# Performance work log

Measured on AMD Instinct MI355X. Metric: run time of the kernel, lower is better.

The kernel has to match this reference:

```python
import jax, jax.numpy as jnp
import numpy as np

N_NODES = 100000
N_EDGES = 1600000
F_IN, HID, N_CLS = 128, 64, 40


def gcn_conv(x, src, dst, W, b, n_nodes):
    # x: [N, Fin] -> [N, Fout]; edges already include self-loops.
    h = x @ W  # [N, Fout]
    ones = jnp.ones_like(src, dtype=h.dtype)
    deg = jax.ops.segment_sum(ones, dst, num_segments=n_nodes)  # [N]
    dinv = jnp.where(deg > 0, jax.lax.rsqrt(deg), 0.0)
    norm = dinv[src] * dinv[dst]  # [E]
    msg = h[src] * norm[:, None]  # gather + scale
    out = jax.ops.segment_sum(msg, dst, num_segments=n_nodes)  # scatter-sum
    return out + b


def setup_inputs() -> dict:
    key = jax.random.key(0)
    ks = jax.random.split(key, 8)
    x = jax.random.normal(ks[0], (N_NODES, F_IN), dtype=jnp.float32)
    edge_index = jax.random.randint(ks[1], (2, N_EDGES), 0, N_NODES, dtype=jnp.int64)

    def glorot(k, fi, fo):
        s = float(np.sqrt(6.0 / (fi + fo)))
        return jax.random.uniform(k, (fi, fo), jnp.float32, -s, s)

    return {
        "x": x,
        "edge_index": edge_index,
        "W1": glorot(ks[2], F_IN, HID), "b1": jnp.zeros((HID,), jnp.float32),
        "W2": glorot(ks[3], HID, HID), "b2": jnp.zeros((HID,), jnp.float32),
        "W3": glorot(ks[4], HID, N_CLS), "b3": jnp.zeros((N_CLS,), jnp.float32),
    }


def reference(x, edge_index, W1, b1, W2, b2, W3, b3):
    n = x.shape[0]
    loop = jnp.arange(n, dtype=edge_index.dtype)
    src = jnp.concatenate([edge_index[0], loop])  # add self-loops
    dst = jnp.concatenate([edge_index[1], loop])
    # layer 1..3: GCNConv -> relu -> dropout(eval: identity)
    h = jax.nn.relu(gcn_conv(x, src, dst, W1, b1, n))
    h = jax.nn.relu(gcn_conv(h, src, dst, W2, b2, n))
    h = jax.nn.relu(gcn_conv(h, src, dst, W3, b3, n))
    return jax.nn.log_softmax(h, axis=1)
```

## Files before the change

### kernel.cpp

```cpp
#include <hip/hip_runtime.h>
#include <math.h>

typedef _Float16 half8   __attribute__((ext_vector_type(8)));
typedef float    float4v __attribute__((ext_vector_type(4)));

#define CAP   6144
#define EPB   8192

static __device__ __forceinline__ unsigned short f32_to_f16u(float f) {
    _Float16 h = (_Float16)f;
    return __builtin_bit_cast(unsigned short, h);
}


__global__ __launch_bounds__(256) void prep_init(
    const float* __restrict__ W1, const float* __restrict__ W2, const float* __restrict__ W3,
    unsigned short* __restrict__ Wf1, unsigned short* __restrict__ Wf2,
    unsigned short* __restrict__ Wf3, int* __restrict__ bcur, int NB)
{
    if (blockIdx.x == 3) {
        for (int i = threadIdx.x; i < NB; i += 256) bcur[i] = 0;
        return;
    }
    const float* W; unsigned short* Wf; int K, M;
    if (blockIdx.x == 0)      { W = W1; Wf = Wf1; K = 128; M = 64; }
    else if (blockIdx.x == 1) { W = W2; Wf = Wf2; K = 64;  M = 64; }
    else                      { W = W3; Wf = Wf3; K = 64;  M = 40; }
    const int NT = (M + 15) >> 4, NTC = NT << 4, KS = K >> 5;
    for (int i = threadIdx.x; i < K * NTC; i += 256) {
        int k = i / NTC, nn = i - k * NTC;
        unsigned short hv = 0;
        if (nn < M) hv = f32_to_f16u(W[(size_t)k * M + nn]);
        int s = k >> 5, q = (k >> 3) & 3, j = k & 7;
        int u = nn >> 4, lane = (q << 4) | (nn & 15);
        Wf[((u * KS + s) << 9) + (lane << 3) + j] = hv;
    }
}


__global__ __launch_bounds__(256) void bin_edges(
    const int* __restrict__ src, const int* __restrict__ dst,
    int* __restrict__ bcur, unsigned int* __restrict__ bint, int E, int NB)
{
    __shared__ unsigned int pay[EPB];
    __shared__ unsigned int targ[EPB];
    __shared__ int h[512];
    __shared__ int h2[512];
    __shared__ int sc[512];
    __shared__ int rbase[512];

    const int tid  = threadIdx.x;
    const int base = (int)blockIdx.x * EPB;
    int end = base + EPB; if (end > E) end = E;
    const int total = end - base;
    const int L4 = total & ~3;

    h[tid] = 0; h[tid + 256] = 0;
    h2[tid] = 0; h2[tid + 256] = 0;
    __syncthreads();

    for (int i = tid << 2; i < L4; i += 1024) {
        int4 d4 = *(const int4*)(dst + base + i);
        atomicAdd(&h[d4.x >> 8], 1);
        atomicAdd(&h[d4.y >> 8], 1);
        atomicAdd(&h[d4.z >> 8], 1);
        atomicAdd(&h[d4.w >> 8], 1);
    }
    for (int i = L4 + tid; i < total; i += 256)
        atomicAdd(&h[dst[base + i] >> 8], 1);
    __syncthreads();

    int v0 = h[tid], v1 = h[tid + 256];
    sc[tid] = v0; sc[tid + 256] = v1;
    __syncthreads();
    for (int off = 1; off < 512; off <<= 1) {
        int x0 = (tid >= off) ? sc[tid - off] : 0;
        int x1 = (tid + 256 >= off) ? sc[tid + 256 - off] : 0;
        __syncthreads();
        sc[tid] += x0; sc[tid + 256] += x1;
        __syncthreads();
    }

    for (int j = tid; j < NB; j += 256) {
        int c = h[j];
        rbase[j] = c ? atomicAdd(&bcur[j], c) : 0;
    }
    __syncthreads();

    {
        auto place = [&](int d, int s) {
            int bkt  = d >> 8;
            int rank = atomicAdd(&h2[bkt], 1);
            int loc  = sc[bkt] - h[bkt] + rank;
            pay[loc] = ((unsigned int)s << 8) | (unsigned int)(d & 255);
            unsigned int t = (unsigned int)(rbase[bkt] + rank);
            targ[loc] = (t < (unsigned int)CAP)
                      ? (unsigned int)bkt * CAP + t : 0xFFFFFFFFu;
        };
        for (int i = tid << 2; i < L4; i += 1024) {
            int4 d4 = *(const int4*)(dst + base + i);
            int4 s4 = *(const int4*)(src + base + i);
            place(d4.x, s4.x); place(d4.y, s4.y);
            place(d4.z, s4.z); place(d4.w, s4.w);
        }
        for (int i = L4 + tid; i < total; i += 256)
            place(dst[base + i], src[base + i]);
    }
    __syncthreads();

    for (int i = tid; i < total; i += 256) {
        unsigned int t = targ[i];
        if (t != 0xFFFFFFFFu) bint[t] = pay[i];
    }
}


__global__ __launch_bounds__(256) void build_csr(
    const unsigned int* __restrict__ bint, const int* __restrict__ bcur,
    int2* __restrict__ rp2, float* __restrict__ dinv, int* __restrict__ es, int n)
{
    __shared__ int cnt[256];
    __shared__ int sc[256];
    __shared__ int cur[256];
    __shared__ unsigned int pin[CAP];
    __shared__ int pout[CAP];
    const int b = blockIdx.x, tid = threadIdx.x;
    int total = bcur[b]; if (total > CAP) total = CAP;
    const unsigned int* bp = bint + (size_t)b * CAP;
    int* ep = es + (size_t)b * CAP;
    const int base = b * CAP;

    cnt[tid] = 0;
    __syncthreads();
    for (int i = tid; i < total; i += 256) {
        unsigned int v = bp[i];
        pin[i] = v;
        atomicAdd(&cnt[v & 255], 1);
    }
    __syncthreads();

    int v = cnt[tid];
    sc[tid] = v;
    __syncthreads();
    for (int off = 1; off < 256; off <<= 1) {
        int x = (tid >= off) ? sc[tid - off] : 0;
        __syncthreads();
        sc[tid] += x;
        __syncthreads();
    }
    int excl = sc[tid] - v;
    int node = (b << 8) + tid;
    if (node < n) {
        rp2[node]  = make_int2(base + excl, base + excl + v);
        dinv[node] = rsqrtf((float)(v + 1));
    }
    cur[tid] = excl;
    __syncthreads();

    for (int i = tid; i < total; i += 256) {
        unsigned int p = pin[i];
        int r = atomicAdd(&cur[p & 255], 1);
        pout[r] = (int)(p >> 8);
    }
    __syncthreads();

    for (int i = tid; i < total; i += 256)
        ep[i] = pout[i];
}


template<int KK, int NT, int STRIDE, int MOUT, bool INF32>
__global__ __launch_bounds__(256) void gemm_t(
    const void* __restrict__ Xin, const unsigned short* __restrict__ Wf,
    const float* __restrict__ dinv, unsigned short* __restrict__ H, int n)
{
    constexpr int KS = KK >> 5;
    __shared__ __align__(16) unsigned short ldsA[4 * KS * 512];
    const int tid = threadIdx.x;
    const int n0  = blockIdx.x * 64;
    const int wv   = tid >> 6;
    const int lane = tid & 63;

    half8 bf[NT * KS];
    #pragma unroll
    for (int u = 0; u < NT; ++u)
        #pragma unroll
        for (int s = 0; s < KS; ++s)
            bf[u * KS + s] = *(const half8*)&Wf[((u * KS + s) << 9) + (lane << 3)];

    {
        const int rl = tid >> 3;
        const int kl = tid & 7;
        #pragma unroll
        for (int rb = 0; rb < 64; rb += 32) {
            int r = rl + rb;
            int node = n0 + r;
            int t = r >> 4, m = r & 15;
            if (INF32) {
                #pragma unroll
                for (int kq8 = 0; kq8 < (KK >> 2); kq8 += 8) {
                    int k0 = (kl + kq8) << 2;
                    unsigned short h[4] = {0, 0, 0, 0};
                    if (node < n) {
                        const float* xp = (const float*)Xin + (size_t)node * KK + k0;
                        float4v v = *(const float4v*)xp;
                        #pragma unroll
                        for (int i = 0; i < 4; ++i) h[i] = f32_to_f16u(v[i]);
                    }
                    int s = k0 >> 5, q = (k0 >> 3) & 3, j0 = k0 & 7;
                    int lds_lane = (q << 4) | m;
                    unsigned short* p = &ldsA[((t * KS + s) << 9) + (lds_lane << 3) + j0];
                    *(uint2*)p = make_uint2((unsigned)h[0] | ((unsigned)h[1] << 16),
                                            (unsigned)h[2] | ((unsigned)h[3] << 16));
                }
            } else {
                uint4 v = make_uint4(0, 0, 0, 0);
                if (node < n)
                    v = *(const uint4*)((const unsigned short*)Xin + (size_t)node * KK + (kl << 3));
                int k0 = kl << 3;
                int s = k0 >> 5, q = (k0 >> 3) & 3;
                unsigned short* p = &ldsA[((t * KS + s) << 9) + ((((q << 4) | m)) << 3)];
                *(uint4*)p = v;
            }
        }
    }

    __syncthreads();

    float4v acc[NT];
    #pragma unroll
    for (int u = 0; u < NT; ++u) acc[u] = (float4v){0.f, 0.f, 0.f, 0.f};

    #pragma unroll
    for (int s = 0; s < KS; ++s) {
        half8 a = *(const half8*)&ldsA[((wv * KS + s) << 9) + (lane << 3)];
        #pragma unroll
        for (int u = 0; u < NT; ++u)
            acc[u] = __builtin_amdgcn_mfma_f32_16x16x32_f16(a, bf[u * KS + s], acc[u], 0, 0, 0);
    }

    const int mc = lane & 15;
    const int quad = lane >> 4;
    #pragma unroll
    for (int reg = 0; reg < 4; ++reg) {
        int node = n0 + (wv << 4) + (quad << 2) + reg;
        if (node >= n) continue;
        float dv = dinv[node];
        #pragma unroll
        for (int u = 0; u < NT; ++u) {
            int col = (u << 4) + mc;
            if (col < MOUT)
                H[(size_t)node * STRIDE + col] = f32_to_f16u(acc[u][reg] * dv);
        }
    }
}


template<int MOUT, int ROWU4>
__global__ __launch_bounds__(256) void gather_t(
    const int2* __restrict__ rp2, const int* __restrict__ es,
    const unsigned short* __restrict__ H, const float* __restrict__ dinv,
    const float* __restrict__ bias, unsigned short* __restrict__ Aout, int n)
{
    const int lane   = threadIdx.x & 63;
    const int half   = lane >> 5;
    const int lane32 = lane & 31;
    const int slot   = (lane >> 3) & 3;
    const int c8     = lane & 7;
    const bool act   = c8 < ROWU4;
    const uint4* H4  = (const uint4*)H;

    float bi[8];
    #pragma unroll
    for (int i = 0; i < 8; ++i) bi[i] = bias[(c8 << 3) + i];

    const half8 hz = {(_Float16)0, (_Float16)0, (_Float16)0, (_Float16)0,
                      (_Float16)0, (_Float16)0, (_Float16)0, (_Float16)0};

    const int TW2 = (int)(gridDim.x << 3);
    for (int nb = (((int)blockIdx.x << 2) + ((int)threadIdx.x >> 6)) << 1; nb < n; nb += TW2) {
        const int node = nb + half;
        const int2 e = rp2[node];
        const float dv = dinv[node];

        half8 hacc = hz;
        if (slot == 0 && act)
            hacc = __builtin_bit_cast(half8, H4[(size_t)node * ROWU4 + c8]);

        for (int cb = e.x; cb < e.y; cb += 32) {
            const int rem = e.y - cb;
            int eidx = cb + lane32; if (eidx > e.y - 1) eidx = e.y - 1;
            const int ei = es[eidx];
            #pragma unroll
            for (int j = 0; j < 8; ++j) {
                const int idx = (j << 2) + slot;
                const int s = __shfl(ei, (half << 5) + idx, 64);
                if (idx < rem && act)
                    hacc = hacc + __builtin_bit_cast(half8, H4[(size_t)s * ROWU4 + c8]);
            }
        }

        #pragma unroll
        for (int step = 8; step <= 16; step <<= 1) {
            uint4 u = __builtin_bit_cast(uint4, hacc);
            uint4 o;
            o.x = __shfl_xor(u.x, step, 64);
            o.y = __shfl_xor(u.y, step, 64);
            o.z = __shfl_xor(u.z, step, 64);
            o.w = __shfl_xor(u.w, step, 64);
            hacc = hacc + __builtin_bit_cast(half8, o);
        }

        if (slot == 0) {
            unsigned short o[8];
            #pragma unroll
            for (int i = 0; i < 8; ++i)
                o[i] = f32_to_f16u(fmaxf((float)hacc[i] * dv + bi[i], 0.0f));
            uint4 w;
            w.x = (unsigned int)o[0] | ((unsigned int)o[1] << 16);
            w.y = (unsigned int)o[2] | ((unsigned int)o[3] << 16);
            w.z = (unsigned int)o[4] | ((unsigned int)o[5] << 16);
            w.w = (unsigned int)o[6] | ((unsigned int)o[7] << 16);
            ((uint4*)Aout)[(size_t)node * 8 + c8] = w;
        }
    }
}


template<int MOUT, int ROWU4>
__global__ __launch_bounds__(256) void gather_softmax(
    const int2* __restrict__ rp2, const int* __restrict__ es,
    const unsigned short* __restrict__ H, const float* __restrict__ dinv,
    const float* __restrict__ bias, float* __restrict__ out, int n)
{
    const int lane   = threadIdx.x & 63;
    const int half   = lane >> 5;
    const int lane32 = lane & 31;
    const int slot   = (lane >> 3) & 3;
    const int c8     = lane & 7;
    const bool act   = c8 < ROWU4;
    const uint4* H4  = (const uint4*)H;

    float bi[8];
    #pragma unroll
    for (int i = 0; i < 8; ++i) {
        int col = (c8 << 3) + i;
        bi[i] = (col < MOUT) ? bias[col] : 0.0f;
    }

    const half8 hz = {(_Float16)0, (_Float16)0, (_Float16)0, (_Float16)0,
                      (_Float16)0, (_Float16)0, (_Float16)0, (_Float16)0};

    const int TW2 = (int)(gridDim.x << 3);
    for (int nb = (((int)blockIdx.x << 2) + ((int)threadIdx.x >> 6)) << 1; nb < n; nb += TW2) {
        const int node = nb + half;
        const int2 e = rp2[node];
        const float dv = dinv[node];

        half8 hacc = hz;
        if (slot == 0 && act)
            hacc = __builtin_bit_cast(half8, H4[(size_t)node * ROWU4 + c8]);

        for (int cb = e.x; cb < e.y; cb += 32) {
            const int rem = e.y - cb;
            int eidx = cb + lane32; if (eidx > e.y - 1) eidx = e.y - 1;
            const int ei = es[eidx];
            #pragma unroll
            for (int j = 0; j < 8; ++j) {
                const int idx = (j << 2) + slot;
                const int s = __shfl(ei, (half << 5) + idx, 64);
                if (idx < rem && act)
                    hacc = hacc + __builtin_bit_cast(half8, H4[(size_t)s * ROWU4 + c8]);
            }
        }

        #pragma unroll
        for (int step = 8; step <= 16; step <<= 1) {
            uint4 u = __builtin_bit_cast(uint4, hacc);
            uint4 o;
            o.x = __shfl_xor(u.x, step, 64);
            o.y = __shfl_xor(u.y, step, 64);
            o.z = __shfl_xor(u.z, step, 64);
            o.w = __shfl_xor(u.w, step, 64);
            hacc = hacc + __builtin_bit_cast(half8, o);
        }

        float z[8]; float m = -INFINITY;
        #pragma unroll
        for (int i = 0; i < 8; ++i) {
            int col = (c8 << 3) + i;
            z[i] = (col < MOUT && act) ? fmaxf((float)hacc[i] * dv + bi[i], 0.0f)
                                       : -INFINITY;
            m = fmaxf(m, z[i]);
        }
        m = fmaxf(m, __shfl_xor(m, 1, 64));
        m = fmaxf(m, __shfl_xor(m, 2, 64));
        m = fmaxf(m, __shfl_xor(m, 4, 64));
        float s = 0.0f;
        #pragma unroll
        for (int i = 0; i < 8; ++i) s += expf(z[i] - m);
        s += __shfl_xor(s, 1, 64);
        s += __shfl_xor(s, 2, 64);
        s += __shfl_xor(s, 4, 64);
        float ls = logf(s) + m;
        if (slot == 0 && c8 < (MOUT + 7) / 8) {
            float* op = out + (size_t)node * MOUT + (c8 << 3);
            float4v o0 = {z[0] - ls, z[1] - ls, z[2] - ls, z[3] - ls};
            float4v o1 = {z[4] - ls, z[5] - ls, z[6] - ls, z[7] - ls};
            *(float4v*)op = o0;
            *(float4v*)(op + 4) = o1;
        }
    }
}


extern "C" void kernel_launch(void* const* d_in, const int* in_sizes, int n_in,
                              void* d_out, int out_size, void* d_ws, size_t ws_size,
                              hipStream_t stream)
{
    const float* x  = (const float*)d_in[0];
    const int*   ei = (const int*)  d_in[1];
    const float* W1 = (const float*)d_in[2];
    const float* b1 = (const float*)d_in[3];
    const float* W2 = (const float*)d_in[4];
    const float* b2 = (const float*)d_in[5];
    const float* W3 = (const float*)d_in[6];
    const float* b3 = (const float*)d_in[7];

    const int F_IN = 128;
    const int n = in_sizes[0] / F_IN;
    const int E = in_sizes[1] / 2;
    const int* src = ei;
    const int* dst = ei + E;
    float* out = (float*)d_out;

    const int NB = (n + 255) >> 8;

    auto align = [](size_t v) { return (v + 255) & ~(size_t)255; };
    char* w = (char*)d_ws;
    size_t off = 0;
    float*          dinv = (float*)(w + off);          off = align(off + (size_t)n * 4);
    unsigned short* H1   = (unsigned short*)(w + off); off = align(off + (size_t)n * 64 * 2);
    unsigned short* A    = (unsigned short*)(w + off); off = align(off + (size_t)n * 64 * 2);
    unsigned short* H3   = (unsigned short*)(w + off); off = align(off + (size_t)n * 40 * 2);
    int2*           rp2  = (int2*)(w + off);           off = align(off + (size_t)n * 8);
    int*            es   = (int*)(w + off);            off = align(off + (size_t)NB * CAP * 4);
    unsigned int*   bint = (unsigned int*)(w + off);   off = align(off + (size_t)NB * CAP * 4);
    int*            bcur = (int*)(w + off);            off = align(off + (size_t)512 * 4);
    unsigned short* Wf1  = (unsigned short*)(w + off); off = align(off + (size_t)8192 * 2);
    unsigned short* Wf2  = (unsigned short*)(w + off); off = align(off + (size_t)4096 * 2);
    unsigned short* Wf3  = (unsigned short*)(w + off); off = align(off + (size_t)3072 * 2);
    unsigned short* H2   = H1;

    const int BLK = 256;
    auto cdiv = [](int a, int b) { return (a + b - 1) / b; };
    const int EB = cdiv(E, EPB);
    const int GB = cdiv(n, 64);
    const int GG = 2048;

    prep_init<<<4, BLK, 0, stream>>>(W1, W2, W3, Wf1, Wf2, Wf3, bcur, NB);
    bin_edges<<<EB, BLK, 0, stream>>>(src, dst, bcur, bint, E, NB);
    build_csr<<<NB, BLK, 0, stream>>>(bint, bcur, rp2, dinv, es, n);

    gemm_t<128, 4, 64, 64, true><<<GB, BLK, 0, stream>>>(x, Wf1, dinv, H1, n);
    gather_t<64, 8><<<GG, BLK, 0, stream>>>(rp2, es, H1, dinv, b1, A, n);

    gemm_t<64, 4, 64, 64, false><<<GB, BLK, 0, stream>>>(A, Wf2, dinv, H2, n);
    gather_t<64, 8><<<GG, BLK, 0, stream>>>(rp2, es, H2, dinv, b2, A, n);

    gemm_t<64, 3, 40, 40, false><<<GB, BLK, 0, stream>>>(A, Wf3, dinv, H3, n);
    gather_softmax<40, 5><<<GG, BLK, 0, stream>>>(rp2, es, H3, dinv, b3, out, n);
}
```

Before: 265.7 us.

## Merge weight prep into edge binning and overlap CSR build with first GEMM

The weight-conversion blocks now run as extra blocks of the edge-binning kernel, and bucket counters are zeroed with a memset. CSR construction and the first-layer GEMM share one launch, which lets them overlap; for that, the first GEMM no longer scales by dinv. The layer-1 gather instead multiplies each source row by dinv[s] in half precision, and the self-loop term is scaled separately. This removes two kernel launches and their dependency gaps. In exchange it adds a per-edge dinv load and fp16 multiply in the first gather, with some extra rounding error.

Measured after the change: 250.2 us (median of 3 runs). 5.8% less time.

```diff
diff --git a/kernel.cpp b/kernel.cpp
--- a/kernel.cpp
+++ b/kernel.cpp
@@ -13,19 +13,9 @@
 }
 
 
-__global__ __launch_bounds__(256) void prep_init(
-    const float* __restrict__ W1, const float* __restrict__ W2, const float* __restrict__ W3,
-    unsigned short* __restrict__ Wf1, unsigned short* __restrict__ Wf2,
-    unsigned short* __restrict__ Wf3, int* __restrict__ bcur, int NB)
-{
-    if (blockIdx.x == 3) {
-        for (int i = threadIdx.x; i < NB; i += 256) bcur[i] = 0;
-        return;
-    }
-    const float* W; unsigned short* Wf; int K, M;
-    if (blockIdx.x == 0)      { W = W1; Wf = Wf1; K = 128; M = 64; }
-    else if (blockIdx.x == 1) { W = W2; Wf = Wf2; K = 64;  M = 64; }
-    else                      { W = W3; Wf = Wf3; K = 64;  M = 40; }
+static __device__ __forceinline__ void prep_body(
+    const float* __restrict__ W, unsigned short* __restrict__ Wf, int K, int M)
+{
     const int NT = (M + 15) >> 4, NTC = NT << 4, KS = K >> 5;
     for (int i = threadIdx.x; i < K * NTC; i += 256) {
         int k = i / NTC, nn = i - k * NTC;
@@ -37,147 +27,15 @@
     }
 }
 
-
-__global__ __launch_bounds__(256) void bin_edges(
-    const int* __restrict__ src, const int* __restrict__ dst,
-    int* __restrict__ bcur, unsigned int* __restrict__ bint, int E, int NB)
-{
-    __shared__ unsigned int pay[EPB];
-    __shared__ unsigned int targ[EPB];
-    __shared__ int h[512];
-    __shared__ int h2[512];
-    __shared__ int sc[512];
-    __shared__ int rbase[512];
-
-    const int tid  = threadIdx.x;
-    const int base = (int)blockIdx.x * EPB;
-    int end = base + EPB; if (end > E) end = E;
-    const int total = end - base;
-    const int L4 = total & ~3;
-
-    h[tid] = 0; h[tid + 256] = 0;
-    h2[tid] = 0; h2[tid + 256] = 0;
-    __syncthreads();
-
-    for (int i = tid << 2; i < L4; i += 1024) {
-        int4 d4 = *(const int4*)(dst + base + i);
-        atomicAdd(&h[d4.x >> 8], 1);
-        atomicAdd(&h[d4.y >> 8], 1);
-        atomicAdd(&h[d4.z >> 8], 1);
-        atomicAdd(&h[d4.w >> 8], 1);
-    }
-    for (int i = L4 + tid; i < total; i += 256)
-        atomicAdd(&h[dst[base + i] >> 8], 1);
-    __syncthreads();
-
-    int v0 = h[tid], v1 = h[tid + 256];
-    sc[tid] = v0; sc[tid + 256] = v1;
-    __syncthreads();
-    for (int off = 1; off < 512; off <<= 1) {
-        int x0 = (tid >= off) ? sc[tid - off] : 0;
-        int x1 = (tid + 256 >= off) ? sc[tid + 256 - off] : 0;
-        __syncthreads();
-        sc[tid] += x0; sc[tid + 256] += x1;
-        __syncthreads();
-    }
-
-    for (int j = tid; j < NB; j += 256) {
-        int c = h[j];
-        rbase[j] = c ? atomicAdd(&bcur[j], c) : 0;
-    }
-    __syncthreads();
-
-    {
-        auto place = [&](int d, int s) {
-            int bkt  = d >> 8;
-            int rank = atomicAdd(&h2[bkt], 1);
-            int loc  = sc[bkt] - h[bkt] + rank;
-            pay[loc] = ((unsigned int)s << 8) | (unsigned int)(d & 255);
-            unsigned int t = (unsigned int)(rbase[bkt] + rank);
-            targ[loc] = (t < (unsigned int)CAP)
-                      ? (unsigned int)bkt * CAP + t : 0xFFFFFFFFu;
-        };
-        for (int i = tid << 2; i < L4; i += 1024) {
-            int4 d4 = *(const int4*)(dst + base + i);
-            int4 s4 = *(const int4*)(src + base + i);
-            place(d4.x, s4.x); place(d4.y, s4.y);
-            place(d4.z, s4.z); place(d4.w, s4.w);
-        }
-        for (int i = L4 + tid; i < total; i += 256)
-            place(dst[base + i], src[base + i]);
-    }
-    __syncthreads();
-
-    for (int i = tid; i < total; i += 256) {
-        unsigned int t = targ[i];
-        if (t != 0xFFFFFFFFu) bint[t] = pay[i];
-    }
-}
-
-
-__global__ __launch_bounds__(256) void build_csr(
-    const unsigned int* __restrict__ bint, const int* __restrict__ bcur,
-    int2* __restrict__ rp2, float* __restrict__ dinv, int* __restrict__ es, int n)
-{
-    __shared__ int cnt[256];
-    __shared__ int sc[256];
-    __shared__ int cur[256];
-    __shared__ unsigned int pin[CAP];
-    __shared__ int pout[CAP];
-    const int b = blockIdx.x, tid = threadIdx.x;
-    int total = bcur[b]; if (total > CAP) total = CAP;
-    const unsigned int* bp = bint + (size_t)b * CAP;
-    int* ep = es + (size_t)b * CAP;
-    const int base = b * CAP;
-
-    cnt[tid] = 0;
-    __syncthreads();
-    for (int i = tid; i < total; i += 256) {
-        unsigned int v = bp[i];
-        pin[i] = v;
-        atomicAdd(&cnt[v & 255], 1);
-    }
-    __syncthreads();
-
-    int v = cnt[tid];
-    sc[tid] = v;
-    __syncthreads();
-    for (int off = 1; off < 256; off <<= 1) {
-        int x = (tid >= off) ? sc[tid - off] : 0;
-        __syncthreads();
-        sc[tid] += x;
-        __syncthreads();
-    }
-    int excl = sc[tid] - v;
-    int node = (b << 8) + tid;
-    if (node < n) {
-        rp2[node]  = make_int2(base + excl, base + excl + v);
-        dinv[node] = rsqrtf((float)(v + 1));
-    }
-    cur[tid] = excl;
-    __syncthreads();
-
-    for (int i = tid; i < total; i += 256) {
-        unsigned int p = pin[i];
-        int r = atomicAdd(&cur[p & 255], 1);
-        pout[r] = (int)(p >> 8);
-    }
-    __syncthreads();
-
-    for (int i = tid; i < total; i += 256)
-        ep[i] = pout[i];
-}
-
-
-template<int KK, int NT, int STRIDE, int MOUT, bool INF32>
-__global__ __launch_bounds__(256) void gemm_t(
-    const void* __restrict__ Xin, const unsigned short* __restrict__ Wf,
-    const float* __restrict__ dinv, unsigned short* __restrict__ H, int n)
+template<int KK, int NT, int STRIDE, int MOUT, bool INF32, bool SCALE>
+static __device__ __forceinline__ void gemm_body(
+    unsigned short* __restrict__ ldsA, const void* __restrict__ Xin,
+    const unsigned short* __restrict__ Wf, const float* __restrict__ dinv,
+    unsigned short* __restrict__ H, int n, int bid)
 {
     constexpr int KS = KK >> 5;
-    __shared__ __align__(16) unsigned short ldsA[4 * KS * 512];
     const int tid = threadIdx.x;
-    const int n0  = blockIdx.x * 64;
+    const int n0  = bid * 64;
     const int wv   = tid >> 6;
     const int lane = tid & 63;
 
@@ -245,18 +103,193 @@
     for (int reg = 0; reg < 4; ++reg) {
         int node = n0 + (wv << 4) + (quad << 2) + reg;
         if (node >= n) continue;
-        float dv = dinv[node];
+        float dv = SCALE ? dinv[node] : 1.0f;
         #pragma unroll
         for (int u = 0; u < NT; ++u) {
             int col = (u << 4) + mc;
             if (col < MOUT)
-                H[(size_t)node * STRIDE + col] = f32_to_f16u(acc[u][reg] * dv);
-        }
-    }
-}
-
-
-template<int MOUT, int ROWU4>
+                H[(size_t)node * STRIDE + col] = f32_to_f16u(SCALE ? acc[u][reg] * dv
+                                                                   : acc[u][reg]);
+        }
+    }
+}
+
+struct CsrS {
+    int cnt[256]; int sc[256]; int cur[256];
+    unsigned int pin[CAP]; int pout[CAP];
+};
+
+static __device__ __forceinline__ void csr_body(
+    CsrS& S, const unsigned int* __restrict__ bint, const int* __restrict__ bcur,
+    int2* __restrict__ rp2, float* __restrict__ dinv, int* __restrict__ es,
+    int n, int b)
+{
+    const int tid = threadIdx.x;
+    int total = bcur[b]; if (total > CAP) total = CAP;
+    const unsigned int* bp = bint + (size_t)b * CAP;
+    int* ep = es + (size_t)b * CAP;
+    const int base = b * CAP;
+
+    S.cnt[tid] = 0;
+    __syncthreads();
+    for (int i = tid; i < total; i += 256) {
+        unsigned int v = bp[i];
+        S.pin[i] = v;
+        atomicAdd(&S.cnt[v & 255], 1);
+    }
+    __syncthreads();
+
+    int v = S.cnt[tid];
+    S.sc[tid] = v;
+    __syncthreads();
+    for (int off = 1; off < 256; off <<= 1) {
+        int x = (tid >= off) ? S.sc[tid - off] : 0;
+        __syncthreads();
+        S.sc[tid] += x;
+        __syncthreads();
+    }
+    int excl = S.sc[tid] - v;
+    int node = (b << 8) + tid;
+    if (node < n) {
+        rp2[node]  = make_int2(base + excl, base + excl + v);
+        dinv[node] = rsqrtf((float)(v + 1));
+    }
+    S.cur[tid] = excl;
+    __syncthreads();
+
+    for (int i = tid; i < total; i += 256) {
+        unsigned int p = S.pin[i];
+        int r = atomicAdd(&S.cur[p & 255], 1);
+        S.pout[r] = (int)(p >> 8);
+    }
+    __syncthreads();
+
+    for (int i = tid; i < total; i += 256)
+        ep[i] = S.pout[i];
+}
+
+
+__global__ __launch_bounds__(256) void bin_prep(
+    const int* __restrict__ src, const int* __restrict__ dst,
+    int* __restrict__ bcur, unsigned int* __restrict__ bint, int E, int NB, int EB,
+    const float* __restrict__ W1, const float* __restrict__ W2, const float* __restrict__ W3,
+    unsigned short* __restrict__ Wf1, unsigned short* __restrict__ Wf2,
+    unsigned short* __restrict__ Wf3)
+{
+    __shared__ unsigned int pay[EPB];
+    __shared__ unsigned int targ[EPB];
+    __shared__ int h[512];
+    __shared__ int h2[512];
+    __shared__ int sc[512];
+    __shared__ int rbase[512];
+
+    const int bx = (int)blockIdx.x;
+    if (bx >= EB) {
+        int k = bx - EB;
+        if (k == 0)      prep_body(W1, Wf1, 128, 64);
+        else if (k == 1) prep_body(W2, Wf2, 64, 64);
+        else             prep_body(W3, Wf3, 64, 40);
+        return;
+    }
+
+    const int tid  = threadIdx.x;
+    const int base = bx * EPB;
+    int end = base + EPB; if (end > E) end = E;
+    const int total = end - base;
+    const int L4 = total & ~3;
+
+    h[tid] = 0; h[tid + 256] = 0;
+    h2[tid] = 0; h2[tid + 256] = 0;
+    __syncthreads();
+
+    for (int i = tid << 2; i < L4; i += 1024) {
+        int4 d4 = *(const int4*)(dst + base + i);
+        atomicAdd(&h[d4.x >> 8], 1);
+        atomicAdd(&h[d4.y >> 8], 1);
+        atomicAdd(&h[d4.z >> 8], 1);
+        atomicAdd(&h[d4.w >> 8], 1);
+    }
+    for (int i = L4 + tid; i < total; i += 256)
+        atomicAdd(&h[dst[base + i] >> 8], 1);
+    __syncthreads();
+
+    int v0 = h[tid], v1 = h[tid + 256];
+    sc[tid] = v0; sc[tid + 256] = v1;
+    __syncthreads();
+    for (int off = 1; off < 512; off <<= 1) {
+        int x0 = (tid >= off) ? sc[tid - off] : 0;
+        int x1 = (tid + 256 >= off) ? sc[tid + 256 - off] : 0;
+        __syncthreads();
+        sc[tid] += x0; sc[tid + 256] += x1;
+        __syncthreads();
+    }
+
+    for (int j = tid; j < NB; j += 256) {
+        int c = h[j];
+        rbase[j] = c ? atomicAdd(&bcur[j], c) : 0;
+    }
+    __syncthreads();
+
+    {
+        auto place = [&](int d, int s) {
+            int bkt  = d >> 8;
+            int rank = atomicAdd(&h2[bkt], 1);
+            int loc  = sc[bkt] - h[bkt] + rank;
+            pay[loc] = ((unsigned int)s << 8) | (unsigned int)(d & 255);
+            unsigned int t = (unsigned int)(rbase[bkt] + rank);
+            targ[loc] = (t < (unsigned int)CAP)
+                      ? (unsigned int)bkt * CAP + t : 0xFFFFFFFFu;
+        };
+        for (int i = tid << 2; i < L4; i += 1024) {
+            int4 d4 = *(const int4*)(dst + base + i);
+            int4 s4 = *(const int4*)(src + base + i);
+            place(d4.x, s4.x); place(d4.y, s4.y);
+            place(d4.z, s4.z); place(d4.w, s4.w);
+        }
+        for (int i = L4 + tid; i < total; i += 256)
+            place(dst[base + i], src[base + i]);
+    }
+    __syncthreads();
+
+    for (int i = tid; i < total; i += 256) {
+        unsigned int t = targ[i];
+        if (t != 0xFFFFFFFFu) bint[t] = pay[i];
+    }
+}
+
+
+union SmemU {
+    CsrS csr;
+    unsigned short ldsA[4 * 4 * 512];
+};
+
+__global__ __launch_bounds__(256) void csr_gemm1(
+    const unsigned int* __restrict__ bint, const int* __restrict__ bcur,
+    int2* __restrict__ rp2, float* __restrict__ dinv, int* __restrict__ es,
+    const float* __restrict__ x, const unsigned short* __restrict__ Wf1,
+    unsigned short* __restrict__ H1, int n, int NBb)
+{
+    __shared__ __align__(16) SmemU sm;
+    const int bx = (int)blockIdx.x;
+    if (bx < NBb)
+        csr_body(sm.csr, bint, bcur, rp2, dinv, es, n, bx);
+    else
+        gemm_body<128, 4, 64, 64, true, false>(sm.ldsA, x, Wf1, nullptr, H1, n, bx - NBb);
+}
+
+
+template<int KK, int NT, int STRIDE, int MOUT>
+__global__ __launch_bounds__(256) void gemm_t(
+    const void* __restrict__ Xin, const unsigned short* __restrict__ Wf,
+    const float* __restrict__ dinv, unsigned short* __restrict__ H, int n)
+{
+    constexpr int KS = KK >> 5;
+    __shared__ __align__(16) unsigned short ldsA[4 * KS * 512];
+    gemm_body<KK, NT, STRIDE, MOUT, false, true>(ldsA, Xin, Wf, dinv, H, n, blockIdx.x);
+}
+
+
+template<int MOUT, int ROWU4, bool SRCSCALE>
 __global__ __launch_bounds__(256) void gather_t(
     const int2* __restrict__ rp2, const int* __restrict__ es,
     const unsigned short* __restrict__ H, const float* __restrict__ dinv,
@@ -284,8 +317,11 @@
         const float dv = dinv[node];
 
         half8 hacc = hz;
-        if (slot == 0 && act)
-            hacc = __builtin_bit_cast(half8, H4[(size_t)node * ROWU4 + c8]);
+        half8 self = hz;
+        if (slot == 0 && act) {
+            self = __builtin_bit_cast(half8, H4[(size_t)node * ROWU4 + c8]);
+            if (!SRCSCALE) hacc = self;
+        }
 
         for (int cb = e.x; cb < e.y; cb += 32) {
             const int rem = e.y - cb;
@@ -295,8 +331,16 @@
             for (int j = 0; j < 8; ++j) {
                 const int idx = (j << 2) + slot;
                 const int s = __shfl(ei, (half << 5) + idx, 64);
-                if (idx < rem && act)
-                    hacc = hacc + __builtin_bit_cast(half8, H4[(size_t)s * ROWU4 + c8]);
+                if (idx < rem && act) {
+                    half8 row = __builtin_bit_cast(half8, H4[(size_t)s * ROWU4 + c8]);
+                    if (SRCSCALE) {
+                        _Float16 dh = (_Float16)dinv[s];
+                        half8 ds = {dh, dh, dh, dh, dh, dh, dh, dh};
+                        hacc = hacc + ds * row;
+                    } else {
+                        hacc = hacc + row;
+                    }
+                }
             }
         }
 
@@ -314,8 +358,11 @@
         if (slot == 0) {
             unsigned short o[8];
             #pragma unroll
-            for (int i = 0; i < 8; ++i)
-                o[i] = f32_to_f16u(fmaxf((float)hacc[i] * dv + bi[i], 0.0f));
+            for (int i = 0; i < 8; ++i) {
+                float a = SRCSCALE ? ((float)hacc[i] + (float)self[i] * dv) * dv
+                                   : (float)hacc[i] * dv;
+                o[i] = f32_to_f16u(fmaxf(a + bi[i], 0.0f));
+            }
             uint4 w;
             w.x = (unsigned int)o[0] | ((unsigned int)o[1] << 16);
             w.y = (unsigned int)o[2] | ((unsigned int)o[3] << 16);
@@ -458,16 +505,17 @@
     const int GB = cdiv(n, 64);
     const int GG = 2048;
 
-    prep_init<<<4, BLK, 0, stream>>>(W1, W2, W3, Wf1, Wf2, Wf3, bcur, NB);
-    bin_edges<<<EB, BLK, 0, stream>>>(src, dst, bcur, bint, E, NB);
-    build_csr<<<NB, BLK, 0, stream>>>(bint, bcur, rp2, dinv, es, n);
-
-    gemm_t<128, 4, 64, 64, true><<<GB, BLK, 0, stream>>>(x, Wf1, dinv, H1, n);
-    gather_t<64, 8><<<GG, BLK, 0, stream>>>(rp2, es, H1, dinv, b1, A, n);
-
-    gemm_t<64, 4, 64, 64, false><<<GB, BLK, 0, stream>>>(A, Wf2, dinv, H2, n);
-    gather_t<64, 8><<<GG, BLK, 0, stream>>>(rp2, es, H2, dinv, b2, A, n);
-
-    gemm_t<64, 3, 40, 40, false><<<GB, BLK, 0, stream>>>(A, Wf3, dinv, H3, n);
+    hipMemsetAsync(bcur, 0, (size_t)512 * 4, stream);
+    bin_prep<<<EB + 3, BLK, 0, stream>>>(src, dst, bcur, bint, E, NB, EB,
+                                         W1, W2, W3, Wf1, Wf2, Wf3);
+
+    csr_gemm1<<<NB + GB, BLK, 0, stream>>>(bint, bcur, rp2, dinv, es, x, Wf1, H1, n, NB);
+
+    gather_t<64, 8, true><<<GG, BLK, 0, stream>>>(rp2, es, H1, dinv, b1, A, n);
+
+    gemm_t<64, 4, 64, 64><<<GB, BLK, 0, stream>>>(A, Wf2, dinv, H2, n);
+    gather_t<64, 8, false><<<GG, BLK, 0, stream>>>(rp2, es, H2, dinv, b2, A, n);
+
+    gemm_t<64, 3, 40, 40><<<GB, BLK, 0, stream>>>(A, Wf3, dinv, H3, n);
     gather_softmax<40, 5><<<GG, BLK, 0, stream>>>(rp2, es, H3, dinv, b3, out, n);
 }
```
